# Kernel tuning notes

Hardware: AMD Instinct MI355X
Metric: run time of the kernel (lower is better)

The kernel has to match this reference:

```python
import jax, jax.numpy as jnp
import numpy as np

E, B, D, T = 8, 4096, 2048, 2048
H = D // 2 + T // 2  # expert hidden dim = 2048
TOP_K = 2


def setup_inputs() -> dict:
    key = jax.random.key(0)
    ks = jax.random.split(key, 5)
    s_in = 1.0 / np.sqrt(D)
    s_h = 1.0 / np.sqrt(H)
    return {
        "xs": jax.random.normal(ks[0], (E, B, D), dtype=jnp.float32),
        "Wg": jax.random.normal(ks[1], (D,), dtype=jnp.float32) * s_in,
        "bg": jnp.zeros((1,), dtype=jnp.float32),
        "W1": jax.random.normal(ks[2], (E, D, H), dtype=jnp.float32) * s_in,
        "b1": jnp.zeros((E, H), dtype=jnp.float32),
        "W2": jax.random.normal(ks[3], (E, H, T), dtype=jnp.float32) * s_h,
        "b2": jnp.zeros((E, T), dtype=jnp.float32),
    }


def reference(xs, Wg, bg, W1, b1, W2, b2):
    # Gating: logits[b, e] = x[e][b] @ Wg + bg  -> [B, E]
    logits = jnp.einsum("ebd,d->be", xs, Wg) + bg
    probs = jax.nn.softmax(logits, axis=1)
    top_k_values, top_k_indices = jax.lax.top_k(probs, TOP_K)  # [B, K]

    # Dense expert compute over each expert's own input stream.
    # hidden[e, b, h] = relu(x[e] @ W1[e] + b1[e]); out[e, b, t] = hidden @ W2[e] + b2[e]
    hidden = jax.nn.relu(jnp.einsum("ebd,edh->ebh", xs, W1) + b1[:, None, :])
    expert_out = jnp.einsum("ebh,eht->ebt", hidden, W2) + b2[:, None, :]  # [E, B, T]

    # Gather the top-k experts per token. In the original, masked-dense compute
    # + output mask is mathematically identical to this gather.
    per_token = jnp.transpose(expert_out, (1, 0, 2))  # [B, E, T]
    selected = jnp.take_along_axis(per_token, top_k_indices[:, :, None], axis=1)  # [B, K, T]

    out = jnp.sum(top_k_values[:, :, None] * selected, axis=1)  # [B, T]
    return out, top_k_values
```

## Files before the change

### kernel.cpp

```cpp
#include <hip/hip_runtime.h>
#include <hip/hip_bf16.h>
#include <stdint.h>

#define E_ 8
#define B_ 4096
#define D_ 2048
#define T_ 2048
#define H_ 2048
#define KDIM 2048
#define NDIM 2048
#define ECAP 2048

typedef __attribute__((ext_vector_type(4))) float f32x4;
typedef __attribute__((ext_vector_type(4))) unsigned short u16x4;
typedef __attribute__((ext_vector_type(8))) unsigned short u16x8;
typedef __attribute__((ext_vector_type(8))) __bf16 bf16x8;

__device__ __forceinline__ unsigned short f2bf(float f) {
    __hip_bfloat16 h = __float2bfloat16(f);
    return __builtin_bit_cast(unsigned short, h);
}

__device__ __forceinline__ void gload_lds16(const void* g, void* lds) {
    __builtin_amdgcn_global_load_lds(
        (const __attribute__((address_space(1))) void*)g,
        (__attribute__((address_space(3))) void*)lds, 16, 0, 0);
}

__global__ __launch_bounds__(256) void fused_pre(
    const float* __restrict__ xs, const float* __restrict__ Wg,
    const float* __restrict__ bg,
    const float* __restrict__ W1, const float* __restrict__ W2,
    unsigned short* __restrict__ Wt1, unsigned short* __restrict__ Wt2,
    float* __restrict__ out_topk, int* __restrict__ counts,
    unsigned short* __restrict__ Axf, int* __restrict__ tokf,
    float* __restrict__ probf, int nwt)
{
    const int bid = blockIdx.x;
    const int t = threadIdx.x;

    if (bid < nwt) {
        const int z   = bid >> 10;
        const int rem = bid & 1023;
        const int kb  = ((rem >> 5) & 31) << 6;
        const int nb  = (rem & 31) << 6;
        const int e   = z & 7;
        const float* W = (z >> 3) ? W2 : W1;
        unsigned short* Wt = (z >> 3) ? Wt2 : Wt1;

        __shared__ float tile[64][65];
        const float* src = W + ((size_t)e * KDIM + kb) * NDIM + nb;
        {
            const int kr = t >> 2, nc = (t & 3) * 16;
            #pragma unroll
            for (int j = 0; j < 4; ++j) {
                f32x4 v = __builtin_nontemporal_load(
                    (const f32x4*)(src + (size_t)kr * NDIM + nc + j * 4));
                tile[kr][nc + j*4 + 0] = v.x;
                tile[kr][nc + j*4 + 1] = v.y;
                tile[kr][nc + j*4 + 2] = v.z;
                tile[kr][nc + j*4 + 3] = v.w;
            }
        }
        __syncthreads();
        {
            const int nn = t >> 2, kc = (t & 3) * 16;
            unsigned short wbuf[16];
            #pragma unroll
            for (int j = 0; j < 16; ++j) wbuf[j] = f2bf(tile[kc + j][nn]);
            unsigned short* dst =
                Wt + ((size_t)e * NDIM + nb + nn) * KDIM + kb + kc;
            *(u16x8*)dst       = *(const u16x8*)&wbuf[0];
            *((u16x8*)dst + 1) = *(const u16x8*)&wbuf[8];
        }
        return;
    }

    const int b = bid - nwt;
    const int wave = t >> 6, lane = t & 63;
    __shared__ float red[E_][4];
    __shared__ int sh_i0, sh_i1, sh_p0, sh_p1;

    const f32x4 wg0 = ((const f32x4*)Wg)[t];
    const f32x4 wg1 = ((const f32x4*)Wg)[t + 256];

    f32x4 xa[E_], xb[E_];
    #pragma unroll
    for (int e = 0; e < E_; ++e) {
        const f32x4* xr = (const f32x4*)(xs + ((size_t)e * B_ + b) * D_);
        xa[e] = __builtin_nontemporal_load(&xr[t]);
        xb[e] = __builtin_nontemporal_load(&xr[t + 256]);
        float p = xa[e].x*wg0.x + xa[e].y*wg0.y + xa[e].z*wg0.z + xa[e].w*wg0.w
                + xb[e].x*wg1.x + xb[e].y*wg1.y + xb[e].z*wg1.z + xb[e].w*wg1.w;
        #pragma unroll
        for (int off = 32; off >= 1; off >>= 1) p += __shfl_xor(p, off);
        if (lane == 0) red[e][wave] = p;
    }
    __syncthreads();
    if (t == 0) {
        float pr[E_];
        float mx = -3.0e38f;
        #pragma unroll
        for (int e = 0; e < E_; ++e) {
            pr[e] = red[e][0] + red[e][1] + red[e][2] + red[e][3] + bg[0];
            mx = fmaxf(mx, pr[e]);
        }
        float s = 0.f;
        #pragma unroll
        for (int e = 0; e < E_; ++e) { pr[e] = expf(pr[e] - mx); s += pr[e]; }
        float inv = 1.0f / s;
        #pragma unroll
        for (int e = 0; e < E_; ++e) pr[e] *= inv;
        int i0 = 0;
        #pragma unroll
        for (int e = 1; e < E_; ++e) if (pr[e] > pr[i0]) i0 = e;
        int i1 = (i0 == 0) ? 1 : 0;
        #pragma unroll
        for (int e = 0; e < E_; ++e) { if (e != i0 && pr[e] > pr[i1]) i1 = e; }
        float p0 = pr[i0], p1 = pr[i1];
        out_topk[2*b]   = p0;
        out_topk[2*b+1] = p1;
        int pos0 = atomicAdd(&counts[i0], 1);
        int pos1 = atomicAdd(&counts[i1], 1);
        if (pos0 >= ECAP) pos0 = ECAP - 1;
        if (pos1 >= ECAP) pos1 = ECAP - 1;
        tokf[i0 * ECAP + pos0] = b;  probf[i0 * ECAP + pos0] = p0;
        tokf[i1 * ECAP + pos1] = b;  probf[i1 * ECAP + pos1] = p1;
        sh_i0 = i0; sh_i1 = i1; sh_p0 = pos0; sh_p1 = pos1;
    }
    __syncthreads();
    const int i0 = sh_i0, i1 = sh_i1;
    f32x4 s0a = xa[0], s0b = xb[0], s1a = xa[0], s1b = xb[0];
    #pragma unroll
    for (int e = 0; e < E_; ++e) {
        if (i0 == e) { s0a = xa[e]; s0b = xb[e]; }
        if (i1 == e) { s1a = xa[e]; s1b = xb[e]; }
    }
    unsigned short* r0 = Axf + (size_t)(i0 * ECAP + sh_p0) * D_;
    unsigned short* r1 = Axf + (size_t)(i1 * ECAP + sh_p1) * D_;
    u16x4 w;
    w[0]=f2bf(s0a.x); w[1]=f2bf(s0a.y); w[2]=f2bf(s0a.z); w[3]=f2bf(s0a.w);
    *(u16x4*)(r0 + 4*t) = w;
    w[0]=f2bf(s0b.x); w[1]=f2bf(s0b.y); w[2]=f2bf(s0b.z); w[3]=f2bf(s0b.w);
    *(u16x4*)(r0 + 1024 + 4*t) = w;
    w[0]=f2bf(s1a.x); w[1]=f2bf(s1a.y); w[2]=f2bf(s1a.z); w[3]=f2bf(s1a.w);
    *(u16x4*)(r1 + 4*t) = w;
    w[0]=f2bf(s1b.x); w[1]=f2bf(s1b.y); w[2]=f2bf(s1b.z); w[3]=f2bf(s1b.w);
    *(u16x4*)(r1 + 1024 + 4*t) = w;
}

__global__ __launch_bounds__(256) void wtrans1(
    const float* __restrict__ W, unsigned short* __restrict__ Wt)
{
    const int e  = blockIdx.z;
    const int kb = blockIdx.x * 64;
    const int nb = blockIdx.y * 64;
    const int t  = threadIdx.x;
    __shared__ float tile[64][65];

    const float* src = W + ((size_t)e * KDIM + kb) * NDIM + nb;
    {
        const int kr = t >> 2, nc = (t & 3) * 16;
        #pragma unroll
        for (int j = 0; j < 4; ++j) {
            f32x4 v = __builtin_nontemporal_load(
                (const f32x4*)(src + (size_t)kr * NDIM + nc + j * 4));
            tile[kr][nc + j*4 + 0] = v.x;
            tile[kr][nc + j*4 + 1] = v.y;
            tile[kr][nc + j*4 + 2] = v.z;
            tile[kr][nc + j*4 + 3] = v.w;
        }
    }
    __syncthreads();
    {
        const int nn = t >> 2, kc = (t & 3) * 16;
        unsigned short wbuf[16];
        #pragma unroll
        for (int j = 0; j < 16; ++j) wbuf[j] = f2bf(tile[kc + j][nn]);
        unsigned short* dst = Wt + ((size_t)e * NDIM + nb + nn) * KDIM + kb + kc;
        *(u16x8*)dst       = *(const u16x8*)&wbuf[0];
        *((u16x8*)dst + 1) = *(const u16x8*)&wbuf[8];
    }
}

#define BAR  __builtin_amdgcn_s_barrier()

template<int LAYER>
__global__ __launch_bounds__(1024, 4) void moe_gemm(
    const unsigned short* __restrict__ Abuf,
    const unsigned short* __restrict__ Wt,
    const float* __restrict__ bias,
    const int* __restrict__ counts,
    const int* __restrict__ tokf,
    const float* __restrict__ probf,
    unsigned short* __restrict__ hidden_out,
    float* __restrict__ out)
{
    const int bid = blockIdx.x;
    const int mt  = bid >> 3;
    const int np  = bid & 7;

    int nMt = 0, base = 0;
    int e = -1, mloc = 0, eb = 0, n_e = 0;
    #pragma unroll
    for (int ee = 0; ee < E_; ++ee) {
        int ce = counts[ee]; if (ce > ECAP) ce = ECAP;
        int te = (ce + 255) >> 8;
        if (e < 0 && mt < nMt + te) {
            e = ee; mloc = (mt - nMt) * 256; eb = base; n_e = ce;
        }
        nMt += te;
        base += ce;
    }
    if (mt >= nMt) return;

    const int arow0 = (LAYER == 1) ? (e * ECAP + mloc) : (eb + mloc);
    const int n0 = np * 256;

    const int t = threadIdx.x;
    const int lane = t & 63;
    const int w = t >> 6;
    const int wm = (w >> 2) * 64;
    const int wn = (w & 3) * 64;
    const int lg = lane >> 4;

    __shared__ u16x8 As[4 * 1024];
    __shared__ u16x8 Bs[4 * 1024];

    const int ksw = (((t & 3) ^ ((t >> 3) & 3)) << 3);
    const unsigned short* aptr = Abuf + (size_t)(arow0 + (t >> 2)) * KDIM + ksw;
    const unsigned short* bptr =
        Wt + ((size_t)e * NDIM + n0 + (t >> 2)) * KDIM + ksw;

#define STG(BUF, KT) do{ \
    gload_lds16(aptr + (KT)*32, &As[(BUF)*1024 + w*64]); \
    gload_lds16(bptr + (KT)*32, &Bs[(BUF)*1024 + w*64]); }while(0)

    f32x4 acc[4][4];
    #pragma unroll
    for (int i = 0; i < 4; ++i)
        #pragma unroll
        for (int j = 0; j < 4; ++j) {
            f32x4 z = {0.f, 0.f, 0.f, 0.f};
            acc[i][j] = z;
        }

    STG(0, 0); STG(1, 1); STG(2, 2);

    const int usw = (lane >> 1) & 3;
    for (int kt = 0; kt < 64; ++kt) {
        asm volatile("s_waitcnt vmcnt(4)" ::: "memory");
        BAR;
        int tn = kt + 3; if (tn > 63) tn = 63;
        STG((kt + 3) & 3, tn);

        const int bse = (kt & 3) * 1024;
        bf16x8 af[4];
        #pragma unroll
        for (int mi = 0; mi < 4; ++mi) {
            const int row = wm + mi * 16 + (lane & 15);
            af[mi] = __builtin_bit_cast(bf16x8, As[bse + row * 4 + (lg ^ usw)]);
        }
        #pragma unroll
        for (int ni = 0; ni < 4; ++ni) {
            const int row = wn + ni * 16 + (lane & 15);
            bf16x8 bq = __builtin_bit_cast(bf16x8, Bs[bse + row * 4 + (lg ^ usw)]);
            #pragma unroll
            for (int mi = 0; mi < 4; ++mi)
                acc[mi][ni] = __builtin_amdgcn_mfma_f32_16x16x32_bf16(
                    af[mi], bq, acc[mi][ni], 0, 0, 0);
        }
    }
    asm volatile("s_waitcnt vmcnt(0)" ::: "memory");

    #pragma unroll
    for (int mi = 0; mi < 4; ++mi) {
        #pragma unroll
        for (int rr = 0; rr < 4; ++rr) {
            const int rloc = wm + mi * 16 + ((lane >> 4) << 2) + rr;
            if (mloc + rloc >= n_e) continue;
            #pragma unroll
            for (int ni = 0; ni < 4; ++ni) {
                const int col = n0 + wn + ni * 16 + (lane & 15);
                float v = acc[mi][ni][rr];
                if (LAYER == 1) {
                    v += bias[e * NDIM + col];
                    v = fmaxf(v, 0.f);
                    hidden_out[(size_t)(eb + mloc + rloc) * H_ + col] = f2bf(v);
                } else {
                    const int f = e * ECAP + mloc + rloc;
                    v = (v + bias[e * NDIM + col]) * probf[f];
                    atomicAdd(&out[(size_t)tokf[f] * T_ + col], v);
                }
            }
        }
    }
#undef STG
}

extern "C" void kernel_launch(void* const* d_in, const int* in_sizes, int n_in,
                              void* d_out, int out_size, void* d_ws, size_t ws_size,
                              hipStream_t stream)
{
    const float* xs = (const float*)d_in[0];
    const float* Wg = (const float*)d_in[1];
    const float* bg = (const float*)d_in[2];
    const float* W1 = (const float*)d_in[3];
    const float* b1 = (const float*)d_in[4];
    const float* W2 = (const float*)d_in[5];
    const float* b2 = (const float*)d_in[6];

    float* out      = (float*)d_out;
    float* out_topk = out + (size_t)B_ * T_;

    char* ws = (char*)d_ws;
    int*   counts = (int*)ws;
    int*   tokf   = (int*)(ws + 1024);
    float* probf  = (float*)(ws + 1024 + E_ * ECAP * 4);
    size_t off = 1024 + (size_t)E_ * ECAP * 8;
    off = (off + 255) & ~(size_t)255;
    unsigned short* Axf    = (unsigned short*)(ws + off); off += (size_t)E_ * ECAP * D_ * 2;
    unsigned short* hidden = (unsigned short*)(ws + off); off += (size_t)(2 * B_ + 256) * H_ * 2;
    unsigned short* Wt1    = (unsigned short*)(ws + off); off += (size_t)E_ * KDIM * NDIM * 2;
    size_t off_big = off + (size_t)E_ * KDIM * NDIM * 2;
    unsigned short* Wt2 = (unsigned short*)(ws + off);

    const bool big = (ws_size >= off_big);

    hipMemsetAsync(counts, 0, 256, stream);
    hipMemsetAsync(out, 0, (size_t)B_ * T_ * sizeof(float), stream);

    dim3 blk(256), gblk(1024);
    dim3 ggrid(39 * 8);

    if (big) {
        const int nwt = 16 * 1024;
        fused_pre<<<dim3(nwt + B_), blk, 0, stream>>>(
            xs, Wg, bg, W1, W2, Wt1, Wt2, out_topk, counts, Axf, tokf, probf, nwt);
        moe_gemm<1><<<ggrid, gblk, 0, stream>>>(
            Axf, Wt1, b1, counts, tokf, probf, hidden, nullptr);
        moe_gemm<2><<<ggrid, gblk, 0, stream>>>(
            hidden, Wt2, b2, counts, tokf, probf, nullptr, out);
    } else {
        dim3 tgrid(32, 32, E_);
        fused_pre<<<dim3(B_), blk, 0, stream>>>(
            xs, Wg, bg, W1, W2, Wt1, Wt1, out_topk, counts, Axf, tokf, probf, 0);
        wtrans1<<<tgrid, blk, 0, stream>>>(W1, Wt1);
        moe_gemm<1><<<ggrid, gblk, 0, stream>>>(
            Axf, Wt1, b1, counts, tokf, probf, hidden, nullptr);
        wtrans1<<<tgrid, blk, 0, stream>>>(W2, Wt1);
        moe_gemm<2><<<ggrid, gblk, 0, stream>>>(
            hidden, Wt1, b2, counts, tokf, probf, nullptr, out);
    }
}
```

Baseline: 493.8 us.

## Overlap W2 transpose-to-bf16 with layer-1 GEMM via extra blocks

The W2 transpose and bf16 conversion moves out of the pre-processing kernel into extra 1024-thread blocks appended to the layer-1 GEMM launch. Each extra block handles eight 64x64 tiles, reusing the GEMM's LDS as a scratch tile. The goal is to hide the W2 conversion's memory traffic behind the layer-1 GEMM, which is mostly compute-bound, and to shorten the pre-processing kernel. The risk is that the transpose blocks, with two barriers per tile, compete with the GEMM blocks for CUs and bandwidth. They may also get scheduled unevenly relative to the GEMM tiles.

```diff
diff --git a/kernel.cpp b/kernel.cpp
--- a/kernel.cpp
+++ b/kernel.cpp
@@ -10,6 +10,7 @@
 #define KDIM 2048
 #define NDIM 2048
 #define ECAP 2048
+#define GEMM_BLKS (39 * 8)
 
 typedef __attribute__((ext_vector_type(4))) float f32x4;
 typedef __attribute__((ext_vector_type(4))) unsigned short u16x4;
@@ -30,8 +31,8 @@
 __global__ __launch_bounds__(256) void fused_pre(
     const float* __restrict__ xs, const float* __restrict__ Wg,
     const float* __restrict__ bg,
-    const float* __restrict__ W1, const float* __restrict__ W2,
-    unsigned short* __restrict__ Wt1, unsigned short* __restrict__ Wt2,
+    const float* __restrict__ W1,
+    unsigned short* __restrict__ Wt1,
     float* __restrict__ out_topk, int* __restrict__ counts,
     unsigned short* __restrict__ Axf, int* __restrict__ tokf,
     float* __restrict__ probf, int nwt)
@@ -40,16 +41,13 @@
     const int t = threadIdx.x;
 
     if (bid < nwt) {
-        const int z   = bid >> 10;
+        const int e   = bid >> 10;
         const int rem = bid & 1023;
         const int kb  = ((rem >> 5) & 31) << 6;
         const int nb  = (rem & 31) << 6;
-        const int e   = z & 7;
-        const float* W = (z >> 3) ? W2 : W1;
-        unsigned short* Wt = (z >> 3) ? Wt2 : Wt1;
 
         __shared__ float tile[64][65];
-        const float* src = W + ((size_t)e * KDIM + kb) * NDIM + nb;
+        const float* src = W1 + ((size_t)e * KDIM + kb) * NDIM + nb;
         {
             const int kr = t >> 2, nc = (t & 3) * 16;
             #pragma unroll
@@ -69,7 +67,7 @@
             #pragma unroll
             for (int j = 0; j < 16; ++j) wbuf[j] = f2bf(tile[kc + j][nn]);
             unsigned short* dst =
-                Wt + ((size_t)e * NDIM + nb + nn) * KDIM + kb + kc;
+                Wt1 + ((size_t)e * NDIM + nb + nn) * KDIM + kb + kc;
             *(u16x8*)dst       = *(const u16x8*)&wbuf[0];
             *((u16x8*)dst + 1) = *(const u16x8*)&wbuf[8];
         }
@@ -194,9 +192,48 @@
     const int* __restrict__ tokf,
     const float* __restrict__ probf,
     unsigned short* __restrict__ hidden_out,
-    float* __restrict__ out)
+    float* __restrict__ out,
+    const float* __restrict__ Wsrc2,
+    unsigned short* __restrict__ Wt2dst,
+    int gemmBlks)
 {
     const int bid = blockIdx.x;
+    const int t = threadIdx.x;
+
+    __shared__ u16x8 As[4 * 1024];
+    __shared__ u16x8 Bs[4 * 1024];
+
+    if (LAYER == 1 && bid >= gemmBlks) {
+        float (*tile)[65] = (float(*)[65])&As[0];
+        const int wb = bid - gemmBlks;
+        #pragma unroll 1
+        for (int i = 0; i < 8; ++i) {
+            const int tau = wb * 8 + i;
+            const int e2  = tau >> 10;
+            const int rem = tau & 1023;
+            const int kb  = ((rem >> 5) & 31) << 6;
+            const int nb  = (rem & 31) << 6;
+            const float* src = Wsrc2 + ((size_t)e2 * KDIM + kb) * NDIM + nb;
+            {
+                const int kr = t >> 4, nc = (t & 15) * 4;
+                f32x4 v = __builtin_nontemporal_load(
+                    (const f32x4*)(src + (size_t)kr * NDIM + nc));
+                tile[kr][nc+0] = v.x; tile[kr][nc+1] = v.y;
+                tile[kr][nc+2] = v.z; tile[kr][nc+3] = v.w;
+            }
+            __syncthreads();
+            {
+                const int nn = t >> 4, kc = (t & 15) * 4;
+                u16x4 wv;
+                wv[0]=f2bf(tile[kc+0][nn]); wv[1]=f2bf(tile[kc+1][nn]);
+                wv[2]=f2bf(tile[kc+2][nn]); wv[3]=f2bf(tile[kc+3][nn]);
+                *(u16x4*)(Wt2dst + ((size_t)e2 * NDIM + nb + nn) * KDIM + kb + kc) = wv;
+            }
+            __syncthreads();
+        }
+        return;
+    }
+
     const int mt  = bid >> 3;
     const int np  = bid & 7;
 
@@ -217,15 +254,11 @@
     const int arow0 = (LAYER == 1) ? (e * ECAP + mloc) : (eb + mloc);
     const int n0 = np * 256;
 
-    const int t = threadIdx.x;
     const int lane = t & 63;
     const int w = t >> 6;
     const int wm = (w >> 2) * 64;
     const int wn = (w & 3) * 64;
     const int lg = lane >> 4;
-
-    __shared__ u16x8 As[4 * 1024];
-    __shared__ u16x8 Bs[4 * 1024];
 
     const int ksw = (((t & 3) ^ ((t >> 3) & 3)) << 3);
     const unsigned short* aptr = Abuf + (size_t)(arow0 + (t >> 2)) * KDIM + ksw;
@@ -331,25 +364,28 @@
     hipMemsetAsync(out, 0, (size_t)B_ * T_ * sizeof(float), stream);
 
     dim3 blk(256), gblk(1024);
-    dim3 ggrid(39 * 8);
 
     if (big) {
-        const int nwt = 16 * 1024;
+        const int nwt = 8 * 1024;
         fused_pre<<<dim3(nwt + B_), blk, 0, stream>>>(
-            xs, Wg, bg, W1, W2, Wt1, Wt2, out_topk, counts, Axf, tokf, probf, nwt);
-        moe_gemm<1><<<ggrid, gblk, 0, stream>>>(
-            Axf, Wt1, b1, counts, tokf, probf, hidden, nullptr);
-        moe_gemm<2><<<ggrid, gblk, 0, stream>>>(
-            hidden, Wt2, b2, counts, tokf, probf, nullptr, out);
+            xs, Wg, bg, W1, Wt1, out_topk, counts, Axf, tokf, probf, nwt);
+        moe_gemm<1><<<dim3(GEMM_BLKS + 1024), gblk, 0, stream>>>(
+            Axf, Wt1, b1, counts, tokf, probf, hidden, nullptr,
+            W2, Wt2, GEMM_BLKS);
+        moe_gemm<2><<<dim3(GEMM_BLKS), gblk, 0, stream>>>(
+            hidden, Wt2, b2, counts, tokf, probf, nullptr, out,
+            nullptr, nullptr, GEMM_BLKS);
     } else {
         dim3 tgrid(32, 32, E_);
         fused_pre<<<dim3(B_), blk, 0, stream>>>(
-            xs, Wg, bg, W1, W2, Wt1, Wt1, out_topk, counts, Axf, tokf, probf, 0);
+            xs, Wg, bg, W1, Wt1, out_topk, counts, Axf, tokf, probf, 0);
         wtrans1<<<tgrid, blk, 0, stream>>>(W1, Wt1);
-        moe_gemm<1><<<ggrid, gblk, 0, stream>>>(
-            Axf, Wt1, b1, counts, tokf, probf, hidden, nullptr);
+        moe_gemm<1><<<dim3(GEMM_BLKS), gblk, 0, stream>>>(
+            Axf, Wt1, b1, counts, tokf, probf, hidden, nullptr,
+            nullptr, nullptr, GEMM_BLKS);
         wtrans1<<<tgrid, blk, 0, stream>>>(W2, Wt1);
-        moe_gemm<2><<<ggrid, gblk, 0, stream>>>(
-            hidden, Wt1, b2, counts, tokf, probf, nullptr, out);
-    }
-}
+        moe_gemm<2><<<dim3(GEMM_BLKS), gblk, 0, stream>>>(
+            hidden, Wt1, b2, counts, tokf, probf, nullptr, out,
+            nullptr, nullptr, GEMM_BLKS);
+    }
+}
```

Measured after the change: 457.6 us. 7.3% less time.
